# Performance work log

Hardware: AMD Instinct MI355X
Metric: run time of the kernel (lower is better)

## Reference

```python
import jax, jax.numpy as jnp
import numpy as np

B, K, U, I, D = 16384, 64, 100000, 100000, 256

def setup_inputs() -> dict:
    key = jax.random.key(0)
    k1, k2, k3, k4, k5, k6, k7, k8 = jax.random.split(key, 8)
    return {
        "nodes_u": jax.random.randint(k1, (B,), 0, U),
        "nodes_v": jax.random.randint(k2, (B,), 0, I),
        "neighbors": jax.random.randint(k3, (B, K), 0, U),
        "neighbor_counts": jax.random.randint(k4, (B,), 0, K + 1),
        "u2e": jax.random.normal(k5, (U, D), dtype=jnp.float32),
        "v2e": jax.random.normal(k6, (I, D), dtype=jnp.float32),
        "W": jax.random.normal(k7, (D, 2 * D), dtype=jnp.float32) * 0.05,  # torch Linear weight [out, in]
        "b": jax.random.normal(k8, (D,), dtype=jnp.float32) * 0.05,
    }

def reference(nodes_u, nodes_v, neighbors, neighbor_counts, u2e, v2e, W, b):
    # self embeddings [B, D]
    self_emb = u2e[nodes_u]
    # gather padded neighbor embeddings [B, K, D]
    neib_emb = u2e[neighbors]
    k_ = neighbors.shape[1]
    mask = jnp.arange(k_)[None, :] < neighbor_counts[:, None]          # [B, K] valid-neighbor mask
    nsum = jnp.einsum('bkd,bk->bd', neib_emb, mask.astype(neib_emb.dtype))
    cnt = jnp.maximum(neighbor_counts, 1).astype(self_emb.dtype)[:, None]
    nmean = nsum / cnt                                                  # mean-pool over valid neighbors
    cat = jnp.concatenate([self_emb, nmean], axis=1)                    # [B, 2D]
    proj = cat @ W.T + b                                                # Linear(2D -> D)
    # users with no neighbors use raw self embedding (matches `if len(neibs) > 0` branch)
    uemb = jnp.where((neighbor_counts > 0)[:, None], proj, self_emb)
    scores = jnp.sum(uemb * v2e[nodes_v], axis=1)                       # [B]
    return scores
```

## Files before the change

### kernel.cpp

```cpp
#include <hip/hip_runtime.h>

#define B_ROWS   16384
#define K_NB     64
#define D_DIM    256
#define TWO_D    512
#define R_BLK    8
#define THREADS  256

__global__ __launch_bounds__(THREADS)
void easyrec_fused(const int* __restrict__ nodes_u,
                   const int* __restrict__ nodes_v,
                   const int* __restrict__ neighbors,
                   const int* __restrict__ neighbor_counts,
                   const float* __restrict__ u2e,
                   const float* __restrict__ v2e,
                   const float* __restrict__ W,
                   const float* __restrict__ bias,
                   float* __restrict__ out)
{
    __shared__ __align__(16) int nbr_lds[R_BLK * K_NB];
    __shared__ __align__(16) float cat_lds[R_BLK][TWO_D];
    __shared__ float red_lds[R_BLK * 4];
    __shared__ float selfdot_lds[R_BLK];
    __shared__ float bdot_lds[R_BLK];

    const int t    = threadIdx.x;
    const int wave = t >> 6;
    const int lane = t & 63;
    const int row0 = blockIdx.x * R_BLK;

    nbr_lds[t]           = neighbors[(size_t)row0 * K_NB + t];
    nbr_lds[t + THREADS] = neighbors[(size_t)row0 * K_NB + t + THREADS];
    __syncthreads();

    for (int rr = 0; rr < 2; ++rr) {
        const int r   = wave + rr * 4;
        const int row = row0 + r;
        const int nu  = __builtin_amdgcn_readfirstlane(nodes_u[row]);
        const int nv  = __builtin_amdgcn_readfirstlane(nodes_v[row]);
        const int cnt = __builtin_amdgcn_readfirstlane(neighbor_counts[row]);

        const float4 self4 = *(const float4*)(u2e + (size_t)nu * D_DIM + 4 * lane);
        const float4 v4    = *(const float4*)(v2e + (size_t)nv * D_DIM + 4 * lane);
        const float4 b4    = *(const float4*)(bias + 4 * lane);

        float4 acc = make_float4(0.f, 0.f, 0.f, 0.f);
        const int base = r * K_NB;
        const int kmax = (cnt + 7) & ~7;
        for (int k = 0; k < kmax; k += 8) {
            const int4 ia = *(const int4*)&nbr_lds[base + k];
            const int4 ib = *(const int4*)&nbr_lds[base + k + 4];
            const float4 n0 = *(const float4*)(u2e + (size_t)ia.x * D_DIM + 4 * lane);
            const float4 n1 = *(const float4*)(u2e + (size_t)ia.y * D_DIM + 4 * lane);
            const float4 n2 = *(const float4*)(u2e + (size_t)ia.z * D_DIM + 4 * lane);
            const float4 n3 = *(const float4*)(u2e + (size_t)ia.w * D_DIM + 4 * lane);
            const float4 n4 = *(const float4*)(u2e + (size_t)ib.x * D_DIM + 4 * lane);
            const float4 n5 = *(const float4*)(u2e + (size_t)ib.y * D_DIM + 4 * lane);
            const float4 n6 = *(const float4*)(u2e + (size_t)ib.z * D_DIM + 4 * lane);
            const float4 n7 = *(const float4*)(u2e + (size_t)ib.w * D_DIM + 4 * lane);
            if (k + 8 <= cnt) {
                acc.x += n0.x + n1.x + n2.x + n3.x + n4.x + n5.x + n6.x + n7.x;
                acc.y += n0.y + n1.y + n2.y + n3.y + n4.y + n5.y + n6.y + n7.y;
                acc.z += n0.z + n1.z + n2.z + n3.z + n4.z + n5.z + n6.z + n7.z;
                acc.w += n0.w + n1.w + n2.w + n3.w + n4.w + n5.w + n6.w + n7.w;
            } else {
                const float m0 = (k + 0 < cnt) ? 1.f : 0.f;
                const float m1 = (k + 1 < cnt) ? 1.f : 0.f;
                const float m2 = (k + 2 < cnt) ? 1.f : 0.f;
                const float m3 = (k + 3 < cnt) ? 1.f : 0.f;
                const float m4 = (k + 4 < cnt) ? 1.f : 0.f;
                const float m5 = (k + 5 < cnt) ? 1.f : 0.f;
                const float m6 = (k + 6 < cnt) ? 1.f : 0.f;
                const float m7 = (k + 7 < cnt) ? 1.f : 0.f;
                acc.x += n0.x*m0 + n1.x*m1 + n2.x*m2 + n3.x*m3 + n4.x*m4 + n5.x*m5 + n6.x*m6 + n7.x*m7;
                acc.y += n0.y*m0 + n1.y*m1 + n2.y*m2 + n3.y*m3 + n4.y*m4 + n5.y*m5 + n6.y*m6 + n7.y*m7;
                acc.z += n0.z*m0 + n1.z*m1 + n2.z*m2 + n3.z*m3 + n4.z*m4 + n5.z*m5 + n6.z*m6 + n7.z*m7;
                acc.w += n0.w*m0 + n1.w*m1 + n2.w*m2 + n3.w*m3 + n4.w*m4 + n5.w*m5 + n6.w*m6 + n7.w*m7;
            }
        }
        const float inv = 1.0f / (float)(cnt > 0 ? cnt : 1);
        float4 nm = make_float4(acc.x * inv, acc.y * inv, acc.z * inv, acc.w * inv);

        *(float4*)(&cat_lds[r][4 * lane])         = self4;
        *(float4*)(&cat_lds[r][D_DIM + 4 * lane]) = nm;

        float sv = self4.x * v4.x + self4.y * v4.y + self4.z * v4.z + self4.w * v4.w;
        float bv = b4.x * v4.x + b4.y * v4.y + b4.z * v4.z + b4.w * v4.w;
        #pragma unroll
        for (int off = 32; off > 0; off >>= 1) {
            sv += __shfl_xor(sv, off, 64);
            bv += __shfl_xor(bv, off, 64);
        }
        if (lane == 0) { selfdot_lds[r] = sv; bdot_lds[r] = bv; }
    }
    __syncthreads();

    const float* vrow[R_BLK];
    #pragma unroll
    for (int r = 0; r < R_BLK; ++r) {
        const int nv = __builtin_amdgcn_readfirstlane(nodes_v[row0 + r]);
        vrow[r] = v2e + (size_t)nv * D_DIM;
    }

    float2 acc2[R_BLK];
    #pragma unroll
    for (int r = 0; r < R_BLK; ++r) acc2[r] = make_float2(0.f, 0.f);

    for (int d = 0; d < D_DIM; d += 4) {
        float4 vq[R_BLK];
        #pragma unroll
        for (int r = 0; r < R_BLK; ++r) vq[r] = *(const float4*)(vrow[r] + d);

        #pragma unroll
        for (int dd = 0; dd < 4; ++dd) {
            const float2 wq = *(const float2*)(W + (size_t)(d + dd) * TWO_D + 2 * t);
            #pragma unroll
            for (int r = 0; r < R_BLK; ++r) {
                const float vs = (dd == 0) ? vq[r].x : (dd == 1) ? vq[r].y
                               : (dd == 2) ? vq[r].z : vq[r].w;
                acc2[r].x += wq.x * vs;
                acc2[r].y += wq.y * vs;
            }
        }
    }

    #pragma unroll
    for (int r = 0; r < R_BLK; ++r) {
        const float2 c2 = *(const float2*)(&cat_lds[r][2 * t]);
        float p = c2.x * acc2[r].x + c2.y * acc2[r].y;
        #pragma unroll
        for (int off = 32; off > 0; off >>= 1) p += __shfl_xor(p, off, 64);
        if (lane == 0) red_lds[r * 4 + wave] = p;
    }
    __syncthreads();

    if (t < R_BLK) {
        const int row = row0 + t;
        const int cnt = neighbor_counts[row];
        float s;
        if (cnt > 0) {
            s = red_lds[t * 4 + 0] + red_lds[t * 4 + 1]
              + red_lds[t * 4 + 2] + red_lds[t * 4 + 3] + bdot_lds[t];
        } else {
            s = selfdot_lds[t];
        }
        out[row] = s;
    }
}

extern "C" void kernel_launch(void* const* d_in, const int* in_sizes, int n_in,
                              void* d_out, int out_size, void* d_ws, size_t ws_size,
                              hipStream_t stream) {
    const int*   nodes_u         = (const int*)d_in[0];
    const int*   nodes_v         = (const int*)d_in[1];
    const int*   neighbors       = (const int*)d_in[2];
    const int*   neighbor_counts = (const int*)d_in[3];
    const float* u2e             = (const float*)d_in[4];
    const float* v2e             = (const float*)d_in[5];
    const float* W               = (const float*)d_in[6];
    const float* bias            = (const float*)d_in[7];
    float*       out             = (float*)d_out;

    const int blocks = B_ROWS / R_BLK;
    easyrec_fused<<<blocks, THREADS, 0, stream>>>(
        nodes_u, nodes_v, neighbors, neighbor_counts, u2e, v2e, W, bias, out);
}
```

Baseline: 316.3 us.

## Precompute W^T v per row and gather bf16 neighbor embeddings

The kernel is restructured so that each block first computes t = W^T v for its 16 rows. The score is then obtained as self·t1 + mean(neighbors)·t2 + b·v, which avoids materialising the concatenated projection. A separate kernel first converts the whole u2e table to bf16 in the workspace, and the neighbor gathers read this half-width copy. That conversion reads and writes the entire 100k-row table on every call, and the bf16 rounding perturbs the neighbor means. The old kernel is kept as a fallback for when the workspace is too small.

```diff
diff --git a/kernel.cpp b/kernel.cpp
--- a/kernel.cpp
+++ b/kernel.cpp
@@ -4,50 +4,196 @@
 #define K_NB     64
 #define D_DIM    256
 #define TWO_D    512
-#define R_BLK    8
+#define U_ROWS   100000
 #define THREADS  256
+#define RB       16
+
+#define WS_NEED  ((size_t)U_ROWS * D_DIM * 2)
 
 __global__ __launch_bounds__(THREADS)
-void easyrec_fused(const int* __restrict__ nodes_u,
-                   const int* __restrict__ nodes_v,
-                   const int* __restrict__ neighbors,
-                   const int* __restrict__ neighbor_counts,
-                   const float* __restrict__ u2e,
-                   const float* __restrict__ v2e,
-                   const float* __restrict__ W,
-                   const float* __restrict__ bias,
-                   float* __restrict__ out)
+void cvt_bf16_kernel(const float* __restrict__ src, unsigned short* __restrict__ dst)
+{
+    const int i = blockIdx.x * THREADS + threadIdx.x;
+    const uint4 u = ((const uint4*)src)[i];
+    ushort4 o;
+    o.x = (unsigned short)((u.x + 0x7FFFu + ((u.x >> 16) & 1u)) >> 16);
+    o.y = (unsigned short)((u.y + 0x7FFFu + ((u.y >> 16) & 1u)) >> 16);
+    o.z = (unsigned short)((u.z + 0x7FFFu + ((u.z >> 16) & 1u)) >> 16);
+    o.w = (unsigned short)((u.w + 0x7FFFu + ((u.w >> 16) & 1u)) >> 16);
+    ((ushort4*)dst)[i] = o;
+}
+
+__device__ inline void bacc(float4& a, uint2 n, float m)
+{
+    union { unsigned u; float f; } c0, c1, c2, c3;
+    c0.u = n.x << 16; c1.u = n.x & 0xFFFF0000u;
+    c2.u = n.y << 16; c3.u = n.y & 0xFFFF0000u;
+    a.x += c0.f * m; a.y += c1.f * m; a.z += c2.f * m; a.w += c3.f * m;
+}
+
+__global__ __launch_bounds__(THREADS, 4)
+void fused_kernel(const int* __restrict__ nodes_u,
+                  const int* __restrict__ nodes_v,
+                  const int* __restrict__ neighbors,
+                  const int* __restrict__ neighbor_counts,
+                  const float* __restrict__ u2e,
+                  const float* __restrict__ v2e,
+                  const float* __restrict__ W,
+                  const float* __restrict__ bias,
+                  const unsigned short* __restrict__ ub,
+                  float* __restrict__ out)
+{
+    __shared__ __align__(16) float v_lds[RB][D_DIM];
+    __shared__ __align__(16) float t2_lds[RB][D_DIM];
+    __shared__ __align__(16) int   nbr_lds[RB * K_NB];
+    __shared__ int   nu_lds[RB];
+    __shared__ float red1[RB][4];
+    __shared__ float red0[RB][4];
+
+    const int t    = threadIdx.x;
+    const int wave = t >> 6;
+    const int lane = t & 63;
+    const int row0 = blockIdx.x * RB;
+
+    #pragma unroll
+    for (int i = 0; i < 4; ++i)
+        nbr_lds[t + THREADS * i] = neighbors[(size_t)row0 * K_NB + t + THREADS * i];
+    if (t < RB) nu_lds[t] = nodes_u[row0 + t];
+    #pragma unroll
+    for (int rr = 0; rr < 4; ++rr) {
+        const int r  = wave + rr * 4;
+        const int nv = __builtin_amdgcn_readfirstlane(nodes_v[row0 + r]);
+        *(float4*)&v_lds[r][4 * lane] = *(const float4*)(v2e + (size_t)nv * D_DIM + 4 * lane);
+    }
+    __syncthreads();
+
+    float2 acc2[RB];
+    #pragma unroll
+    for (int r = 0; r < RB; ++r) acc2[r] = make_float2(0.f, 0.f);
+
+    for (int d = 0; d < D_DIM; d += 4) {
+        const float2 wq0 = *(const float2*)(W + (size_t)(d + 0) * TWO_D + 2 * t);
+        const float2 wq1 = *(const float2*)(W + (size_t)(d + 1) * TWO_D + 2 * t);
+        const float2 wq2 = *(const float2*)(W + (size_t)(d + 2) * TWO_D + 2 * t);
+        const float2 wq3 = *(const float2*)(W + (size_t)(d + 3) * TWO_D + 2 * t);
+        #pragma unroll
+        for (int r = 0; r < RB; ++r) {
+            const float4 vv = *(const float4*)&v_lds[r][d];
+            acc2[r].x += wq0.x * vv.x + wq1.x * vv.y + wq2.x * vv.z + wq3.x * vv.w;
+            acc2[r].y += wq0.y * vv.x + wq1.y * vv.y + wq2.y * vv.z + wq3.y * vv.w;
+        }
+    }
+
+    if (t >= 128) {
+        const int c = 2 * t - 256;
+        #pragma unroll
+        for (int r = 0; r < RB; ++r)
+            *(float2*)&t2_lds[r][c] = acc2[r];
+    }
+    for (int r = 0; r < RB; ++r) {
+        float p1 = 0.f, p0 = 0.f;
+        if (t < 128) {
+            const float2 s2  = *(const float2*)(u2e + (size_t)nu_lds[r] * D_DIM + 2 * t);
+            const float2 vv2 = *(const float2*)&v_lds[r][2 * t];
+            const float2 b2  = *(const float2*)(bias + 2 * t);
+            p1 = s2.x * acc2[r].x + s2.y * acc2[r].y + b2.x * vv2.x + b2.y * vv2.y;
+            p0 = s2.x * vv2.x + s2.y * vv2.y;
+        }
+        #pragma unroll
+        for (int off = 32; off > 0; off >>= 1) {
+            p1 += __shfl_xor(p1, off, 64);
+            p0 += __shfl_xor(p0, off, 64);
+        }
+        if (lane == 0) { red1[r][wave] = p1; red0[r][wave] = p0; }
+    }
+    __syncthreads();
+
+    const int lo = 4 * lane;
+    for (int rr = 0; rr < 4; ++rr) {
+        const int r   = wave + rr * 4;
+        const int row = row0 + r;
+        const int cnt = __builtin_amdgcn_readfirstlane(neighbor_counts[row]);
+
+        const float4 t24 = *(const float4*)&t2_lds[r][lo];
+        float4 acc = make_float4(0.f, 0.f, 0.f, 0.f);
+        const int base = r * K_NB;
+        const int kmax = (cnt + 7) & ~7;
+
+        for (int k = 0; k < kmax; k += 8) {
+            const int4 ia = *(const int4*)&nbr_lds[base + k];
+            const int4 ib = *(const int4*)&nbr_lds[base + k + 4];
+            const int i0 = __builtin_amdgcn_readfirstlane(ia.x);
+            const int i1 = __builtin_amdgcn_readfirstlane(ia.y);
+            const int i2 = __builtin_amdgcn_readfirstlane(ia.z);
+            const int i3 = __builtin_amdgcn_readfirstlane(ia.w);
+            const int i4 = __builtin_amdgcn_readfirstlane(ib.x);
+            const int i5 = __builtin_amdgcn_readfirstlane(ib.y);
+            const int i6 = __builtin_amdgcn_readfirstlane(ib.z);
+            const int i7 = __builtin_amdgcn_readfirstlane(ib.w);
+            const uint2 n0 = *(const uint2*)(ub + (size_t)i0 * D_DIM + lo);
+            const uint2 n1 = *(const uint2*)(ub + (size_t)i1 * D_DIM + lo);
+            const uint2 n2 = *(const uint2*)(ub + (size_t)i2 * D_DIM + lo);
+            const uint2 n3 = *(const uint2*)(ub + (size_t)i3 * D_DIM + lo);
+            const uint2 n4 = *(const uint2*)(ub + (size_t)i4 * D_DIM + lo);
+            const uint2 n5 = *(const uint2*)(ub + (size_t)i5 * D_DIM + lo);
+            const uint2 n6 = *(const uint2*)(ub + (size_t)i6 * D_DIM + lo);
+            const uint2 n7 = *(const uint2*)(ub + (size_t)i7 * D_DIM + lo);
+            if (k + 8 <= cnt) {
+                bacc(acc, n0, 1.f); bacc(acc, n1, 1.f); bacc(acc, n2, 1.f); bacc(acc, n3, 1.f);
+                bacc(acc, n4, 1.f); bacc(acc, n5, 1.f); bacc(acc, n6, 1.f); bacc(acc, n7, 1.f);
+            } else {
+                bacc(acc, n0, (k + 0 < cnt) ? 1.f : 0.f);
+                bacc(acc, n1, (k + 1 < cnt) ? 1.f : 0.f);
+                bacc(acc, n2, (k + 2 < cnt) ? 1.f : 0.f);
+                bacc(acc, n3, (k + 3 < cnt) ? 1.f : 0.f);
+                bacc(acc, n4, (k + 4 < cnt) ? 1.f : 0.f);
+                bacc(acc, n5, (k + 5 < cnt) ? 1.f : 0.f);
+                bacc(acc, n6, (k + 6 < cnt) ? 1.f : 0.f);
+                bacc(acc, n7, (k + 7 < cnt) ? 1.f : 0.f);
+            }
+        }
+
+        float part = acc.x * t24.x + acc.y * t24.y + acc.z * t24.z + acc.w * t24.w;
+        #pragma unroll
+        for (int off = 32; off > 0; off >>= 1) part += __shfl_xor(part, off, 64);
+
+        if (lane == 0) {
+            const float sb = red1[r][0] + red1[r][1] + red1[r][2] + red1[r][3];
+            const float sa = red0[r][0] + red0[r][1] + red0[r][2] + red0[r][3];
+            out[row] = (cnt > 0) ? sb + part * (1.0f / (float)cnt) : sa;
+        }
+    }
+}
+
+#define R_BLK 8
+__global__ __launch_bounds__(THREADS)
+void easyrec_fused_fb(const int* __restrict__ nodes_u, const int* __restrict__ nodes_v,
+                      const int* __restrict__ neighbors, const int* __restrict__ neighbor_counts,
+                      const float* __restrict__ u2e, const float* __restrict__ v2e,
+                      const float* __restrict__ W, const float* __restrict__ bias,
+                      float* __restrict__ out)
 {
     __shared__ __align__(16) int nbr_lds[R_BLK * K_NB];
     __shared__ __align__(16) float cat_lds[R_BLK][TWO_D];
     __shared__ float red_lds[R_BLK * 4];
     __shared__ float selfdot_lds[R_BLK];
     __shared__ float bdot_lds[R_BLK];
-
-    const int t    = threadIdx.x;
-    const int wave = t >> 6;
-    const int lane = t & 63;
+    const int t = threadIdx.x, wave = t >> 6, lane = t & 63;
     const int row0 = blockIdx.x * R_BLK;
-
-    nbr_lds[t]           = neighbors[(size_t)row0 * K_NB + t];
+    nbr_lds[t] = neighbors[(size_t)row0 * K_NB + t];
     nbr_lds[t + THREADS] = neighbors[(size_t)row0 * K_NB + t + THREADS];
     __syncthreads();
-
     for (int rr = 0; rr < 2; ++rr) {
-        const int r   = wave + rr * 4;
-        const int row = row0 + r;
-        const int nu  = __builtin_amdgcn_readfirstlane(nodes_u[row]);
-        const int nv  = __builtin_amdgcn_readfirstlane(nodes_v[row]);
+        const int r = wave + rr * 4, row = row0 + r;
+        const int nu = __builtin_amdgcn_readfirstlane(nodes_u[row]);
+        const int nv = __builtin_amdgcn_readfirstlane(nodes_v[row]);
         const int cnt = __builtin_amdgcn_readfirstlane(neighbor_counts[row]);
-
         const float4 self4 = *(const float4*)(u2e + (size_t)nu * D_DIM + 4 * lane);
-        const float4 v4    = *(const float4*)(v2e + (size_t)nv * D_DIM + 4 * lane);
-        const float4 b4    = *(const float4*)(bias + 4 * lane);
-
+        const float4 v4 = *(const float4*)(v2e + (size_t)nv * D_DIM + 4 * lane);
+        const float4 b4 = *(const float4*)(bias + 4 * lane);
         float4 acc = make_float4(0.f, 0.f, 0.f, 0.f);
-        const int base = r * K_NB;
-        const int kmax = (cnt + 7) & ~7;
-        for (int k = 0; k < kmax; k += 8) {
+        const int base = r * K_NB, km = (cnt + 7) & ~7;
+        for (int k = 0; k < km; k += 8) {
             const int4 ia = *(const int4*)&nbr_lds[base + k];
             const int4 ib = *(const int4*)&nbr_lds[base + k + 4];
             const float4 n0 = *(const float4*)(u2e + (size_t)ia.x * D_DIM + 4 * lane);
@@ -58,72 +204,44 @@
             const float4 n5 = *(const float4*)(u2e + (size_t)ib.y * D_DIM + 4 * lane);
             const float4 n6 = *(const float4*)(u2e + (size_t)ib.z * D_DIM + 4 * lane);
             const float4 n7 = *(const float4*)(u2e + (size_t)ib.w * D_DIM + 4 * lane);
-            if (k + 8 <= cnt) {
-                acc.x += n0.x + n1.x + n2.x + n3.x + n4.x + n5.x + n6.x + n7.x;
-                acc.y += n0.y + n1.y + n2.y + n3.y + n4.y + n5.y + n6.y + n7.y;
-                acc.z += n0.z + n1.z + n2.z + n3.z + n4.z + n5.z + n6.z + n7.z;
-                acc.w += n0.w + n1.w + n2.w + n3.w + n4.w + n5.w + n6.w + n7.w;
-            } else {
-                const float m0 = (k + 0 < cnt) ? 1.f : 0.f;
-                const float m1 = (k + 1 < cnt) ? 1.f : 0.f;
-                const float m2 = (k + 2 < cnt) ? 1.f : 0.f;
-                const float m3 = (k + 3 < cnt) ? 1.f : 0.f;
-                const float m4 = (k + 4 < cnt) ? 1.f : 0.f;
-                const float m5 = (k + 5 < cnt) ? 1.f : 0.f;
-                const float m6 = (k + 6 < cnt) ? 1.f : 0.f;
-                const float m7 = (k + 7 < cnt) ? 1.f : 0.f;
-                acc.x += n0.x*m0 + n1.x*m1 + n2.x*m2 + n3.x*m3 + n4.x*m4 + n5.x*m5 + n6.x*m6 + n7.x*m7;
-                acc.y += n0.y*m0 + n1.y*m1 + n2.y*m2 + n3.y*m3 + n4.y*m4 + n5.y*m5 + n6.y*m6 + n7.y*m7;
-                acc.z += n0.z*m0 + n1.z*m1 + n2.z*m2 + n3.z*m3 + n4.z*m4 + n5.z*m5 + n6.z*m6 + n7.z*m7;
-                acc.w += n0.w*m0 + n1.w*m1 + n2.w*m2 + n3.w*m3 + n4.w*m4 + n5.w*m5 + n6.w*m6 + n7.w*m7;
-            }
+            const float m0 = (k+0<cnt)?1.f:0.f, m1=(k+1<cnt)?1.f:0.f, m2=(k+2<cnt)?1.f:0.f, m3=(k+3<cnt)?1.f:0.f;
+            const float m4 = (k+4<cnt)?1.f:0.f, m5=(k+5<cnt)?1.f:0.f, m6=(k+6<cnt)?1.f:0.f, m7=(k+7<cnt)?1.f:0.f;
+            acc.x += n0.x*m0+n1.x*m1+n2.x*m2+n3.x*m3+n4.x*m4+n5.x*m5+n6.x*m6+n7.x*m7;
+            acc.y += n0.y*m0+n1.y*m1+n2.y*m2+n3.y*m3+n4.y*m4+n5.y*m5+n6.y*m6+n7.y*m7;
+            acc.z += n0.z*m0+n1.z*m1+n2.z*m2+n3.z*m3+n4.z*m4+n5.z*m5+n6.z*m6+n7.z*m7;
+            acc.w += n0.w*m0+n1.w*m1+n2.w*m2+n3.w*m3+n4.w*m4+n5.w*m5+n6.w*m6+n7.w*m7;
         }
         const float inv = 1.0f / (float)(cnt > 0 ? cnt : 1);
-        float4 nm = make_float4(acc.x * inv, acc.y * inv, acc.z * inv, acc.w * inv);
-
-        *(float4*)(&cat_lds[r][4 * lane])         = self4;
-        *(float4*)(&cat_lds[r][D_DIM + 4 * lane]) = nm;
-
-        float sv = self4.x * v4.x + self4.y * v4.y + self4.z * v4.z + self4.w * v4.w;
-        float bv = b4.x * v4.x + b4.y * v4.y + b4.z * v4.z + b4.w * v4.w;
-        #pragma unroll
-        for (int off = 32; off > 0; off >>= 1) {
-            sv += __shfl_xor(sv, off, 64);
-            bv += __shfl_xor(bv, off, 64);
-        }
+        *(float4*)(&cat_lds[r][4 * lane]) = self4;
+        *(float4*)(&cat_lds[r][D_DIM + 4 * lane]) = make_float4(acc.x*inv, acc.y*inv, acc.z*inv, acc.w*inv);
+        float sv = self4.x*v4.x + self4.y*v4.y + self4.z*v4.z + self4.w*v4.w;
+        float bv = b4.x*v4.x + b4.y*v4.y + b4.z*v4.z + b4.w*v4.w;
+        #pragma unroll
+        for (int off = 32; off > 0; off >>= 1) { sv += __shfl_xor(sv, off, 64); bv += __shfl_xor(bv, off, 64); }
         if (lane == 0) { selfdot_lds[r] = sv; bdot_lds[r] = bv; }
     }
     __syncthreads();
-
     const float* vrow[R_BLK];
     #pragma unroll
-    for (int r = 0; r < R_BLK; ++r) {
-        const int nv = __builtin_amdgcn_readfirstlane(nodes_v[row0 + r]);
-        vrow[r] = v2e + (size_t)nv * D_DIM;
-    }
-
+    for (int r = 0; r < R_BLK; ++r)
+        vrow[r] = v2e + (size_t)__builtin_amdgcn_readfirstlane(nodes_v[row0 + r]) * D_DIM;
     float2 acc2[R_BLK];
     #pragma unroll
     for (int r = 0; r < R_BLK; ++r) acc2[r] = make_float2(0.f, 0.f);
-
     for (int d = 0; d < D_DIM; d += 4) {
         float4 vq[R_BLK];
         #pragma unroll
         for (int r = 0; r < R_BLK; ++r) vq[r] = *(const float4*)(vrow[r] + d);
-
         #pragma unroll
         for (int dd = 0; dd < 4; ++dd) {
             const float2 wq = *(const float2*)(W + (size_t)(d + dd) * TWO_D + 2 * t);
             #pragma unroll
             for (int r = 0; r < R_BLK; ++r) {
-                const float vs = (dd == 0) ? vq[r].x : (dd == 1) ? vq[r].y
-                               : (dd == 2) ? vq[r].z : vq[r].w;
-                acc2[r].x += wq.x * vs;
-                acc2[r].y += wq.y * vs;
+                const float vs = (dd==0)?vq[r].x:(dd==1)?vq[r].y:(dd==2)?vq[r].z:vq[r].w;
+                acc2[r].x += wq.x * vs; acc2[r].y += wq.y * vs;
             }
         }
     }
-
     #pragma unroll
     for (int r = 0; r < R_BLK; ++r) {
         const float2 c2 = *(const float2*)(&cat_lds[r][2 * t]);
@@ -133,18 +251,11 @@
         if (lane == 0) red_lds[r * 4 + wave] = p;
     }
     __syncthreads();
-
     if (t < R_BLK) {
-        const int row = row0 + t;
-        const int cnt = neighbor_counts[row];
-        float s;
-        if (cnt > 0) {
-            s = red_lds[t * 4 + 0] + red_lds[t * 4 + 1]
-              + red_lds[t * 4 + 2] + red_lds[t * 4 + 3] + bdot_lds[t];
-        } else {
-            s = selfdot_lds[t];
-        }
-        out[row] = s;
+        const int row = row0 + t, cnt = neighbor_counts[row];
+        out[row] = (cnt > 0)
+            ? red_lds[t*4+0] + red_lds[t*4+1] + red_lds[t*4+2] + red_lds[t*4+3] + bdot_lds[t]
+            : selfdot_lds[t];
     }
 }
 
@@ -161,7 +272,14 @@
     const float* bias            = (const float*)d_in[7];
     float*       out             = (float*)d_out;
 
-    const int blocks = B_ROWS / R_BLK;
-    easyrec_fused<<<blocks, THREADS, 0, stream>>>(
-        nodes_u, nodes_v, neighbors, neighbor_counts, u2e, v2e, W, bias, out);
-}
+    if (ws_size < WS_NEED) {
+        easyrec_fused_fb<<<B_ROWS / R_BLK, THREADS, 0, stream>>>(
+            nodes_u, nodes_v, neighbors, neighbor_counts, u2e, v2e, W, bias, out);
+        return;
+    }
+
+    unsigned short* ub = (unsigned short*)d_ws;
+    cvt_bf16_kernel<<<U_ROWS * D_DIM / 4 / THREADS, THREADS, 0, stream>>>(u2e, ub);
+    fused_kernel<<<B_ROWS / RB, THREADS, 0, stream>>>(
+        nodes_u, nodes_v, neighbors, neighbor_counts, u2e, v2e, W, bias, ub, out);
+}
```

Result: no change. 317.7 us (+0.4%).
